# Kernel optimization log

Measured on AMD Instinct MI355X. Metric: run time of the kernel, lower is better.

## Reference

```python
import jax, jax.numpy as jnp
import numpy as np


def setup_inputs() -> dict:
    key = jax.random.key(0)
    ks = jax.random.split(key, 9)
    B, Q, K, F, C = 16, 2048, 2048, 128, 2
    q = jax.random.normal(ks[0], (B, Q, F), dtype=jnp.float32)
    k = jax.random.normal(ks[1], (B, K, F), dtype=jnp.float32)
    v = jax.random.normal(ks[2], (B, K, F), dtype=jnp.float32)
    coords_q = jax.random.uniform(ks[3], (B, Q, C), dtype=jnp.float32)
    coords_k = jax.random.uniform(ks[4], (B, K, C), dtype=jnp.float32)
    attn_mask = jax.random.randint(ks[5], (B, Q, K), 0, 2).astype(jnp.bool_)
    alibi_mask = jax.random.randint(ks[6], (B, Q, K), 0, 2).astype(jnp.bool_)
    bias_scale = jax.random.uniform(ks[7], (1,), dtype=jnp.float32)  # nn.Parameter(torch.rand(1))
    running_mean = jnp.ones((1,), dtype=jnp.float32)  # RunningMeanScaler buffer (eval mode)
    return {"q": q, "k": k, "v": v, "coords_q": coords_q, "coords_k": coords_k,
            "attn_mask": attn_mask, "alibi_mask": alibi_mask,
            "bias_scale": bias_scale, "running_mean": running_mean}


def reference(q, k, v, coords_q, coords_k, attn_mask, alibi_mask, bias_scale, running_mean):
    # [b,q,k] attention logits
    scale = jnp.asarray(k.shape[-1], q.dtype) ** -0.5
    weight_logits = jnp.einsum('bqf,bkf->bqk', q, k) * scale
    # pairwise coordinate distances [b,q,k]
    diff = coords_q[:, :, None, :] - coords_k[:, None, :, :]
    distances = jnp.sqrt(jnp.sum(diff * diff, axis=-1))
    scaled_distances = (distances / running_mean) * bias_scale  # broadcast scalars
    masked_distances = jnp.where(alibi_mask, jnp.zeros((), distances.dtype), scaled_distances)
    weights = jax.nn.softmax(weight_logits, axis=-1)
    masked = jnp.where(attn_mask, jnp.zeros((), weights.dtype), weights - masked_distances)
    attention = jnp.einsum('bqk,bkf->bqf', masked, v)
    return attention
```

## Files before the change

### kernel.cpp

```cpp
#include <hip/hip_runtime.h>
#include <stdint.h>

#define B_  16
#define QL  2048
#define KL  2048
#define FD  128
#define BQ  64
#define BK  32
#define NSTEP (KL/BK)

#define KSTR  136
#define VTOFF 4352
#define VTSTR 40
#define BUFSHORTS 9472
#define PSTR  40

typedef __attribute__((ext_vector_type(8))) short bf16x8;
typedef __attribute__((ext_vector_type(4))) float f32x4;

__device__ __forceinline__ unsigned short f2b(float f) {
  union { float f; unsigned u; } x; x.f = f;
  return (unsigned short)((x.u + 0x8000u) >> 16);
}

__global__ __launch_bounds__(256, 2) void alibi_attn(
    const float* __restrict__ qp,
    const float* __restrict__ kp,
    const float* __restrict__ vp,
    const float* __restrict__ cqp,
    const float* __restrict__ ckp,
    const int* __restrict__ amp,
    const int* __restrict__ almp,
    const float* __restrict__ bsp,
    const float* __restrict__ rmp,
    float* __restrict__ outp)
{
  __shared__ unsigned short kv[2 * BUFSHORTS];
  __shared__ unsigned short plds[4][2][16 * PSTR];

  const int t    = threadIdx.x;
  const int w    = t >> 6;
  const int lane = t & 63;
  const int l15  = lane & 15;
  const int q4   = lane >> 4;

  const int bid  = blockIdx.x;
  const int xcd  = bid & 7, slot = bid >> 3;
  const int b    = (xcd << 1) | (slot >> 5);
  const int qbase = (slot & 31) * BQ;

  const float bscale = bsp[0] / rmp[0];
  const float sl2 = 0.08838834764831845f * 1.44269504089f;

  const int kr_st = t >> 3;
  const int fb_st = (t & 7) * 4;

  {
    const float* qg = qp + ((long long)(b * QL + qbase)) * FD;
    #pragma unroll
    for (int i = 0; i < 8; ++i) {
      int idx = t + 256 * i;
      float4 u = ((const float4*)qg)[idx];
      int row = idx >> 5, col = (idx & 31) * 4;
      ushort4 s4; s4.x = f2b(u.x); s4.y = f2b(u.y); s4.z = f2b(u.z); s4.w = f2b(u.w);
      *(ushort4*)&kv[row * KSTR + col] = s4;
    }
  }
  __syncthreads();
  bf16x8 qfrag[4];
  {
    const int m = w * 16 + l15;
    #pragma unroll
    for (int fs = 0; fs < 4; ++fs)
      qfrag[fs] = *(const bf16x8*)&kv[m * KSTR + fs * 32 + q4 * 8];
  }
  float cqx[4], cqy[4];
  long long mrow_base[4];
  #pragma unroll
  for (int r = 0; r < 4; ++r) {
    const int qg_ = qbase + w * 16 + q4 * 4 + r;
    float2 c2 = *(const float2*)(cqp + ((long long)(b * QL + qg_)) * 2);
    cqx[r] = c2.x; cqy[r] = c2.y;
    mrow_base[r] = ((long long)(b * QL + qg_)) * KL;
  }
  __syncthreads();

  const float* kgb = kp + ((long long)b * KL) * FD;
  const float* vgb = vp + ((long long)b * KL) * FD;

  int am_b[2][2][4], al_b[2][2][4];
  float ckx_b[2][2], cky_b[2][2];
  #pragma unroll
  for (int s = 0; s < 2; ++s) {
    const int kg = s * 16 + l15;
    #pragma unroll
    for (int r = 0; r < 4; ++r) {
      am_b[0][s][r] = __builtin_nontemporal_load(amp + mrow_base[r] + kg);
      al_b[0][s][r] = __builtin_nontemporal_load(almp + mrow_base[r] + kg);
    }
    float2 c2 = *(const float2*)(ckp + ((long long)(b * KL + kg)) * 2);
    ckx_b[0][s] = c2.x; cky_b[0][s] = c2.y;
  }
  {
    float4 kld[4], vld[4];
    #pragma unroll
    for (int i = 0; i < 4; ++i) {
      kld[i] = *(const float4*)(kgb + (long long)kr_st * FD + fb_st + 32 * i);
      vld[i] = *(const float4*)(vgb + (long long)kr_st * FD + fb_st + 32 * i);
    }
    #pragma unroll
    for (int i = 0; i < 4; ++i) {
      ushort4 s4; s4.x = f2b(kld[i].x); s4.y = f2b(kld[i].y);
      s4.z = f2b(kld[i].z); s4.w = f2b(kld[i].w);
      *(ushort4*)&kv[kr_st * KSTR + fb_st + 32 * i] = s4;
      const int f0 = fb_st + 32 * i;
      kv[VTOFF + (f0 + 0) * VTSTR + kr_st] = f2b(vld[i].x);
      kv[VTOFF + (f0 + 1) * VTSTR + kr_st] = f2b(vld[i].y);
      kv[VTOFF + (f0 + 2) * VTSTR + kr_st] = f2b(vld[i].z);
      kv[VTOFF + (f0 + 3) * VTSTR + kr_st] = f2b(vld[i].w);
    }
  }
  __syncthreads();

  f32x4 O1[8], O2[8];
  #pragma unroll
  for (int n = 0; n < 8; ++n) {
    O1[n] = (f32x4){0.f, 0.f, 0.f, 0.f};
    O2[n] = (f32x4){0.f, 0.f, 0.f, 0.f};
  }
  float lsum[4] = {0.f, 0.f, 0.f, 0.f};

  #pragma unroll 2
  for (int kt = 0; kt < NSTEP; ++kt) {
    const int cur = kt & 1, nxt = cur ^ 1;
    const unsigned short* kb = kv + cur * BUFSHORTS;
    unsigned short*       nb = kv + nxt * BUFSHORTS;
    const int ktp = (kt + 1 < NSTEP) ? (kt + 1) : kt;
    const int k0p = ktp * BK;

    float4 kld[4], vld[4];
    #pragma unroll
    for (int i = 0; i < 4; ++i) {
      kld[i] = *(const float4*)(kgb + (long long)(k0p + kr_st) * FD + fb_st + 32 * i);
      vld[i] = *(const float4*)(vgb + (long long)(k0p + kr_st) * FD + fb_st + 32 * i);
    }
    #pragma unroll
    for (int s = 0; s < 2; ++s) {
      const int kg = k0p + s * 16 + l15;
      #pragma unroll
      for (int r = 0; r < 4; ++r) {
        am_b[nxt][s][r] = __builtin_nontemporal_load(amp + mrow_base[r] + kg);
        al_b[nxt][s][r] = __builtin_nontemporal_load(almp + mrow_base[r] + kg);
      }
      float2 c2 = *(const float2*)(ckp + ((long long)(b * KL + kg)) * 2);
      ckx_b[nxt][s] = c2.x; cky_b[nxt][s] = c2.y;
    }

    f32x4 S0 = (f32x4){0.f, 0.f, 0.f, 0.f};
    f32x4 S1 = (f32x4){0.f, 0.f, 0.f, 0.f};
    #pragma unroll
    for (int fs = 0; fs < 4; ++fs) {
      bf16x8 kb0 = *(const bf16x8*)&kb[(l15)      * KSTR + fs * 32 + q4 * 8];
      bf16x8 kb1 = *(const bf16x8*)&kb[(16 + l15) * KSTR + fs * 32 + q4 * 8];
      S0 = __builtin_amdgcn_mfma_f32_16x16x32_bf16(qfrag[fs], kb0, S0, 0, 0, 0);
      S1 = __builtin_amdgcn_mfma_f32_16x16x32_bf16(qfrag[fs], kb1, S1, 0, 0, 0);
    }

    #pragma unroll
    for (int s = 0; s < 2; ++s) {
      const f32x4 Sv = s ? S1 : S0;
      #pragma unroll
      for (int r = 0; r < 4; ++r) {
        float e = __builtin_amdgcn_exp2f(Sv[r] * sl2);
        lsum[r] += e;
        float dx = cqx[r] - ckx_b[cur][s], dy = cqy[r] - cky_b[cur][s];
        float d  = sqrtf(fmaf(dx, dx, dy * dy)) * bscale;
        int am = am_b[cur][s][r], al = al_b[cur][s][r];
        float wv = am ? 0.f : e;
        float tv = (am | al) ? 0.f : d;
        const int mm = q4 * 4 + r, c = s * 16 + l15;
        plds[w][0][mm * PSTR + c] = f2b(wv);
        plds[w][1][mm * PSTR + c] = f2b(tv);
      }
    }

    bf16x8 aw = *(const bf16x8*)&plds[w][0][l15 * PSTR + q4 * 8];
    bf16x8 at = *(const bf16x8*)&plds[w][1][l15 * PSTR + q4 * 8];
    #pragma unroll
    for (int n = 0; n < 8; ++n) {
      bf16x8 vb = *(const bf16x8*)&kb[VTOFF + (n * 16 + l15) * VTSTR + q4 * 8];
      O1[n] = __builtin_amdgcn_mfma_f32_16x16x32_bf16(aw, vb, O1[n], 0, 0, 0);
      O2[n] = __builtin_amdgcn_mfma_f32_16x16x32_bf16(at, vb, O2[n], 0, 0, 0);
    }

    #pragma unroll
    for (int i = 0; i < 4; ++i) {
      ushort4 s4; s4.x = f2b(kld[i].x); s4.y = f2b(kld[i].y);
      s4.z = f2b(kld[i].z); s4.w = f2b(kld[i].w);
      *(ushort4*)&nb[kr_st * KSTR + fb_st + 32 * i] = s4;
      const int f0 = fb_st + 32 * i;
      nb[VTOFF + (f0 + 0) * VTSTR + kr_st] = f2b(vld[i].x);
      nb[VTOFF + (f0 + 1) * VTSTR + kr_st] = f2b(vld[i].y);
      nb[VTOFF + (f0 + 2) * VTSTR + kr_st] = f2b(vld[i].z);
      nb[VTOFF + (f0 + 3) * VTSTR + kr_st] = f2b(vld[i].w);
    }
    __syncthreads();
  }

  #pragma unroll
  for (int off = 1; off < 16; off <<= 1) {
    #pragma unroll
    for (int r = 0; r < 4; ++r) lsum[r] += __shfl_xor(lsum[r], off, 64);
  }
  float linv[4];
  #pragma unroll
  for (int r = 0; r < 4; ++r) linv[r] = 1.0f / lsum[r];

  #pragma unroll
  for (int n = 0; n < 8; ++n) {
    #pragma unroll
    for (int r = 0; r < 4; ++r) {
      const int qg_ = qbase + w * 16 + q4 * 4 + r;
      const int f   = n * 16 + l15;
      float val = O1[n][r] * linv[r] - O2[n][r];
      __builtin_nontemporal_store(val, outp + ((long long)(b * QL + qg_)) * FD + f);
    }
  }
}

extern "C" void kernel_launch(void* const* d_in, const int* in_sizes, int n_in,
                              void* d_out, int out_size, void* d_ws, size_t ws_size,
                              hipStream_t stream) {
  const float* q   = (const float*)d_in[0];
  const float* k   = (const float*)d_in[1];
  const float* v   = (const float*)d_in[2];
  const float* cq  = (const float*)d_in[3];
  const float* ck  = (const float*)d_in[4];
  const int*   am  = (const int*)d_in[5];
  const int*   alm = (const int*)d_in[6];
  const float* bs  = (const float*)d_in[7];
  const float* rm  = (const float*)d_in[8];
  float*       out = (float*)d_out;

  dim3 grid(B_ * (QL / BQ));
  dim3 block(256);
  hipLaunchKernelGGL(alibi_attn, grid, block, 0, stream,
                     q, k, v, cq, ck, am, alm, bs, rm, out);
}
```

Measured before the change: 676.2 us.

## Vectorize mask loads through packed LDS bytes and swizzle transposed V layout

Mask loads now use 16-byte vector loads per thread covering a 64x32 tile. The two masks are packed into one byte per element in a small shared buffer, replacing 16 scalar int loads per thread per step. The V transpose now loads scalar columns across four keys and writes short4 into an XOR-swizzled layout, replacing the scattered 2-byte LDS stores with fewer, wider ones. The cost is scalar global V loads, extra byte LDS reads in the softmax stage, and split 8-byte reads when building the V fragments.

Measured after the change: 731.5 us. +8.2%, slower.

```diff
diff --git a/kernel.cpp b/kernel.cpp
--- a/kernel.cpp
+++ b/kernel.cpp
@@ -11,12 +11,13 @@
 
 #define KSTR  136
 #define VTOFF 4352
-#define VTSTR 40
-#define BUFSHORTS 9472
+#define BUFS  8448
 #define PSTR  40
+#define MSTR  36
 
 typedef __attribute__((ext_vector_type(8))) short bf16x8;
 typedef __attribute__((ext_vector_type(4))) float f32x4;
+typedef __attribute__((ext_vector_type(4))) int   i32x4;
 
 __device__ __forceinline__ unsigned short f2b(float f) {
   union { float f; unsigned u; } x; x.f = f;
@@ -35,8 +36,9 @@
     const float* __restrict__ rmp,
     float* __restrict__ outp)
 {
-  __shared__ unsigned short kv[2 * BUFSHORTS];
+  __shared__ unsigned short kv[2 * BUFS];
   __shared__ unsigned short plds[4][2][16 * PSTR];
+  __shared__ unsigned char  mlds[2][64 * MSTR];
 
   const int t    = threadIdx.x;
   const int w    = t >> 6;
@@ -52,8 +54,17 @@
   const float bscale = bsp[0] / rmp[0];
   const float sl2 = 0.08838834764831845f * 1.44269504089f;
 
-  const int kr_st = t >> 3;
-  const int fb_st = (t & 7) * 4;
+  const int kr_st = t >> 3, fb_st = (t & 7) * 4;
+  const int vrq = t >> 5, vfc = t & 31;
+  const int vwp = ((vrq ^ ((vfc >> 1) & 7)) * 4);
+  const int vwa = VTOFF + vfc * 32 + vwp;
+  const int mrow = t >> 2, mcol = (t & 3) * 8;
+  const long long mgbase = ((long long)(b * QL + qbase + mrow)) * KL + mcol;
+  const int mlo = mrow * MSTR + mcol;
+  const int sv_r = l15 >> 1;
+  const int voff0 = ((2 * q4) ^ sv_r) * 4;
+  const int voff1 = ((2 * q4 + 1) ^ sv_r) * 4;
+  const int vrb = VTOFF + l15 * 32;
 
   {
     const float* qg = qp + ((long long)(b * QL + qbase)) * FD;
@@ -75,49 +86,57 @@
       qfrag[fs] = *(const bf16x8*)&kv[m * KSTR + fs * 32 + q4 * 8];
   }
   float cqx[4], cqy[4];
-  long long mrow_base[4];
   #pragma unroll
   for (int r = 0; r < 4; ++r) {
     const int qg_ = qbase + w * 16 + q4 * 4 + r;
     float2 c2 = *(const float2*)(cqp + ((long long)(b * QL + qg_)) * 2);
     cqx[r] = c2.x; cqy[r] = c2.y;
-    mrow_base[r] = ((long long)(b * QL + qg_)) * KL;
   }
   __syncthreads();
 
   const float* kgb = kp + ((long long)b * KL) * FD;
   const float* vgb = vp + ((long long)b * KL) * FD;
 
-  int am_b[2][2][4], al_b[2][2][4];
   float ckx_b[2][2], cky_b[2][2];
-  #pragma unroll
-  for (int s = 0; s < 2; ++s) {
-    const int kg = s * 16 + l15;
-    #pragma unroll
-    for (int r = 0; r < 4; ++r) {
-      am_b[0][s][r] = __builtin_nontemporal_load(amp + mrow_base[r] + kg);
-      al_b[0][s][r] = __builtin_nontemporal_load(almp + mrow_base[r] + kg);
-    }
-    float2 c2 = *(const float2*)(ckp + ((long long)(b * KL + kg)) * 2);
-    ckx_b[0][s] = c2.x; cky_b[0][s] = c2.y;
-  }
+
   {
-    float4 kld[4], vld[4];
-    #pragma unroll
-    for (int i = 0; i < 4; ++i) {
+    i32x4 a0 = __builtin_nontemporal_load((const i32x4*)(amp + mgbase));
+    i32x4 a1 = __builtin_nontemporal_load((const i32x4*)(amp + mgbase + 4));
+    i32x4 g0 = __builtin_nontemporal_load((const i32x4*)(almp + mgbase));
+    i32x4 g1 = __builtin_nontemporal_load((const i32x4*)(almp + mgbase + 4));
+    float4 kld[4];
+    float  vsc[4][4];
+    #pragma unroll
+    for (int i = 0; i < 4; ++i)
       kld[i] = *(const float4*)(kgb + (long long)kr_st * FD + fb_st + 32 * i);
-      vld[i] = *(const float4*)(vgb + (long long)kr_st * FD + fb_st + 32 * i);
-    }
+    #pragma unroll
+    for (int d = 0; d < 4; ++d)
+      #pragma unroll
+      for (int kk = 0; kk < 4; ++kk)
+        vsc[d][kk] = vgb[(long long)(4 * vrq + kk) * FD + vfc + 32 * d];
+    #pragma unroll
+    for (int s = 0; s < 2; ++s) {
+      float2 c2 = *(const float2*)(ckp + ((long long)(b * KL + s * 16 + l15)) * 2);
+      ckx_b[0][s] = c2.x; cky_b[0][s] = c2.y;
+    }
+    unsigned ua = (unsigned)(a0[0] | (a0[1] << 8) | (a0[2] << 16) | (a0[3] << 24));
+    unsigned ul = (unsigned)(g0[0] | (g0[1] << 8) | (g0[2] << 16) | (g0[3] << 24));
+    *(unsigned*)&mlds[0][mlo] = ua | (ul << 1);
+    ua = (unsigned)(a1[0] | (a1[1] << 8) | (a1[2] << 16) | (a1[3] << 24));
+    ul = (unsigned)(g1[0] | (g1[1] << 8) | (g1[2] << 16) | (g1[3] << 24));
+    *(unsigned*)&mlds[0][mlo + 4] = ua | (ul << 1);
     #pragma unroll
     for (int i = 0; i < 4; ++i) {
       ushort4 s4; s4.x = f2b(kld[i].x); s4.y = f2b(kld[i].y);
       s4.z = f2b(kld[i].z); s4.w = f2b(kld[i].w);
       *(ushort4*)&kv[kr_st * KSTR + fb_st + 32 * i] = s4;
-      const int f0 = fb_st + 32 * i;
-      kv[VTOFF + (f0 + 0) * VTSTR + kr_st] = f2b(vld[i].x);
-      kv[VTOFF + (f0 + 1) * VTSTR + kr_st] = f2b(vld[i].y);
-      kv[VTOFF + (f0 + 2) * VTSTR + kr_st] = f2b(vld[i].z);
-      kv[VTOFF + (f0 + 3) * VTSTR + kr_st] = f2b(vld[i].w);
+    }
+    #pragma unroll
+    for (int d = 0; d < 4; ++d) {
+      short4 w4;
+      w4.x = (short)f2b(vsc[d][0]); w4.y = (short)f2b(vsc[d][1]);
+      w4.z = (short)f2b(vsc[d][2]); w4.w = (short)f2b(vsc[d][3]);
+      *(short4*)&kv[vwa + 1024 * d] = w4;
     }
   }
   __syncthreads();
@@ -133,26 +152,28 @@
   #pragma unroll 2
   for (int kt = 0; kt < NSTEP; ++kt) {
     const int cur = kt & 1, nxt = cur ^ 1;
-    const unsigned short* kb = kv + cur * BUFSHORTS;
-    unsigned short*       nb = kv + nxt * BUFSHORTS;
+    const unsigned short* kb = kv + cur * BUFS;
+    unsigned short*       nb = kv + nxt * BUFS;
     const int ktp = (kt + 1 < NSTEP) ? (kt + 1) : kt;
     const int k0p = ktp * BK;
 
-    float4 kld[4], vld[4];
-    #pragma unroll
-    for (int i = 0; i < 4; ++i) {
+    i32x4 a0 = __builtin_nontemporal_load((const i32x4*)(amp + mgbase + k0p));
+    i32x4 a1 = __builtin_nontemporal_load((const i32x4*)(amp + mgbase + k0p + 4));
+    i32x4 g0 = __builtin_nontemporal_load((const i32x4*)(almp + mgbase + k0p));
+    i32x4 g1 = __builtin_nontemporal_load((const i32x4*)(almp + mgbase + k0p + 4));
+    float4 kld[4];
+    float  vsc[4][4];
+    #pragma unroll
+    for (int i = 0; i < 4; ++i)
       kld[i] = *(const float4*)(kgb + (long long)(k0p + kr_st) * FD + fb_st + 32 * i);
-      vld[i] = *(const float4*)(vgb + (long long)(k0p + kr_st) * FD + fb_st + 32 * i);
-    }
+    #pragma unroll
+    for (int d = 0; d < 4; ++d)
+      #pragma unroll
+      for (int kk = 0; kk < 4; ++kk)
+        vsc[d][kk] = vgb[(long long)(k0p + 4 * vrq + kk) * FD + vfc + 32 * d];
     #pragma unroll
     for (int s = 0; s < 2; ++s) {
-      const int kg = k0p + s * 16 + l15;
-      #pragma unroll
-      for (int r = 0; r < 4; ++r) {
-        am_b[nxt][s][r] = __builtin_nontemporal_load(amp + mrow_base[r] + kg);
-        al_b[nxt][s][r] = __builtin_nontemporal_load(almp + mrow_base[r] + kg);
-      }
-      float2 c2 = *(const float2*)(ckp + ((long long)(b * KL + kg)) * 2);
+      float2 c2 = *(const float2*)(ckp + ((long long)(b * KL + k0p + s * 16 + l15)) * 2);
       ckx_b[nxt][s] = c2.x; cky_b[nxt][s] = c2.y;
     }
 
@@ -171,13 +192,13 @@
       const f32x4 Sv = s ? S1 : S0;
       #pragma unroll
       for (int r = 0; r < 4; ++r) {
+        unsigned char m = mlds[cur][(w * 16 + q4 * 4 + r) * MSTR + s * 16 + l15];
         float e = __builtin_amdgcn_exp2f(Sv[r] * sl2);
         lsum[r] += e;
         float dx = cqx[r] - ckx_b[cur][s], dy = cqy[r] - cky_b[cur][s];
         float d  = sqrtf(fmaf(dx, dx, dy * dy)) * bscale;
-        int am = am_b[cur][s][r], al = al_b[cur][s][r];
-        float wv = am ? 0.f : e;
-        float tv = (am | al) ? 0.f : d;
+        float wv = (m & 1) ? 0.f : e;
+        float tv = m ? 0.f : d;
         const int mm = q4 * 4 + r, c = s * 16 + l15;
         plds[w][0][mm * PSTR + c] = f2b(wv);
         plds[w][1][mm * PSTR + c] = f2b(tv);
@@ -188,21 +209,33 @@
     bf16x8 at = *(const bf16x8*)&plds[w][1][l15 * PSTR + q4 * 8];
     #pragma unroll
     for (int n = 0; n < 8; ++n) {
-      bf16x8 vb = *(const bf16x8*)&kb[VTOFF + (n * 16 + l15) * VTSTR + q4 * 8];
+      short4 v0 = *(const short4*)&kb[vrb + 512 * n + voff0];
+      short4 v1 = *(const short4*)&kb[vrb + 512 * n + voff1];
+      bf16x8 vb;
+      vb[0] = v0.x; vb[1] = v0.y; vb[2] = v0.z; vb[3] = v0.w;
+      vb[4] = v1.x; vb[5] = v1.y; vb[6] = v1.z; vb[7] = v1.w;
       O1[n] = __builtin_amdgcn_mfma_f32_16x16x32_bf16(aw, vb, O1[n], 0, 0, 0);
       O2[n] = __builtin_amdgcn_mfma_f32_16x16x32_bf16(at, vb, O2[n], 0, 0, 0);
     }
 
+    unsigned ua = (unsigned)(a0[0] | (a0[1] << 8) | (a0[2] << 16) | (a0[3] << 24));
+    unsigned ul = (unsigned)(g0[0] | (g0[1] << 8) | (g0[2] << 16) | (g0[3] << 24));
+    *(unsigned*)&mlds[nxt][mlo] = ua | (ul << 1);
+    ua = (unsigned)(a1[0] | (a1[1] << 8) | (a1[2] << 16) | (a1[3] << 24));
+    ul = (unsigned)(g1[0] | (g1[1] << 8) | (g1[2] << 16) | (g1[3] << 24));
+    *(unsigned*)&mlds[nxt][mlo + 4] = ua | (ul << 1);
     #pragma unroll
     for (int i = 0; i < 4; ++i) {
       ushort4 s4; s4.x = f2b(kld[i].x); s4.y = f2b(kld[i].y);
       s4.z = f2b(kld[i].z); s4.w = f2b(kld[i].w);
       *(ushort4*)&nb[kr_st * KSTR + fb_st + 32 * i] = s4;
-      const int f0 = fb_st + 32 * i;
-      nb[VTOFF + (f0 + 0) * VTSTR + kr_st] = f2b(vld[i].x);
-      nb[VTOFF + (f0 + 1) * VTSTR + kr_st] = f2b(vld[i].y);
-      nb[VTOFF + (f0 + 2) * VTSTR + kr_st] = f2b(vld[i].z);
-      nb[VTOFF + (f0 + 3) * VTSTR + kr_st] = f2b(vld[i].w);
+    }
+    #pragma unroll
+    for (int d = 0; d < 4; ++d) {
+      short4 w4;
+      w4.x = (short)f2b(vsc[d][0]); w4.y = (short)f2b(vsc[d][1]);
+      w4.z = (short)f2b(vsc[d][2]); w4.w = (short)f2b(vsc[d][3]);
+      *(short4*)&nb[vwa + 1024 * d] = w4;
     }
     __syncthreads();
   }
```
